# Optimization experiments

Measured on AMD Instinct MI355X. Metric: run time of the kernel, lower is better.

The kernel has to match this reference:

```python
import jax, jax.numpy as jnp
import numpy as np

TAU = 0.5   # init tau
BN_EPS = 1e-5


def _mlp(x, W1, b1, W2, b2, gamma, beta):
    # NRI MLP: fc -> ELU -> fc -> ELU -> batch-norm over flattened (B*E) rows
    h = jax.nn.elu(x @ W1 + b1)
    h = jax.nn.elu(h @ W2 + b2)
    m = h.mean(axis=(0, 1))
    v = jnp.var(h, axis=(0, 1))
    return gamma * (h - m) * jax.lax.rsqrt(v + BN_EPS) + beta


def setup_inputs() -> dict:
    key = jax.random.key(0)
    B, N, F_IN, FC, H = 16, 128, 8, 256, 256
    E = N * (N - 1)
    ks = jax.random.split(key, 24)

    # fully-connected off-diagonal edge list -> one-hot relation matrices
    pairs = np.array([(i, j) for i in range(N) for j in range(N) if i != j], dtype=np.int64)
    eye = np.eye(N, dtype=np.float32)
    rel_rec = jnp.broadcast_to(jnp.asarray(eye[pairs[:, 0]]), (B, E, N))
    rel_send = jnp.broadcast_to(jnp.asarray(eye[pairs[:, 1]]), (B, E, N))

    graph = jax.random.normal(ks[0], (B, E, F_IN), dtype=jnp.float32)
    u = jax.random.uniform(ks[1], (B, E, F_IN), minval=1e-6, maxval=1.0 - 1e-6)
    gumbel_noise = -jnp.log(-jnp.log(u))

    def lin(k, i, o):
        return jax.random.normal(k, (i, o), dtype=jnp.float32) / np.sqrt(i)

    inp = dict(graph=graph, rel_rec=rel_rec, rel_send=rel_send, gumbel_noise=gumbel_noise,
        m1_W1=lin(ks[2], F_IN, FC), m1_b1=jnp.zeros(FC), m1_W2=lin(ks[3], FC, FC), m1_b2=jnp.zeros(FC),
        m1_g=jnp.ones(FC), m1_beta=jnp.zeros(FC),
        m2_W1=lin(ks[4], FC, FC), m2_b1=jnp.zeros(FC), m2_W2=lin(ks[5], FC, FC), m2_b2=jnp.zeros(FC),
        m2_g=jnp.ones(FC), m2_beta=jnp.zeros(FC),
        Wi=lin(ks[6], 2 * FC, H), bi=jnp.zeros(H), Wn=lin(ks[7], 2 * FC, H), bn_b=jnp.zeros(H),
        f1_W=lin(ks[8], H, H), f1_b=jnp.zeros(H), f2_W=lin(ks[9], H, H), f2_b=jnp.zeros(H),
        f3_W=lin(ks[10], H, F_IN), f3_b=jnp.zeros(F_IN))
    return inp


def reference(graph, rel_rec, rel_send, gumbel_noise,
              m1_W1, m1_b1, m1_W2, m1_b2, m1_g, m1_beta,
              m2_W1, m2_b1, m2_W2, m2_b2, m2_g, m2_beta,
              Wi, bi, Wn, bn_b, f1_W, f1_b, f2_W, f2_b, f3_W, f3_b):
    N = rel_rec.shape[-1]
    # source does graph[:, :, :] = graph[0, 0] (broadcast first edge feature)
    graph = jnp.broadcast_to(graph[0, 0], graph.shape)
    x = _mlp(graph, m1_W1, m1_b1, m1_W2, m1_b2, m1_g, m1_beta)          # [B,E,FC]
    # edge2node: mean aggregation of incoming edges (one-hot matmul == scatter-add / N)
    node = jnp.einsum('ben,bef->bnf', rel_rec, x) / N                    # [B,N,FC]
    node = _mlp(node, m2_W1, m2_b1, m2_W2, m2_b2, m2_g, m2_beta)
    # node2edge: gather receiver/sender node features
    recv = jnp.einsum('ben,bnf->bef', rel_rec, node)
    send = jnp.einsum('ben,bnf->bef', rel_send, node)
    x = jnp.concatenate([recv, send], axis=-1)                           # [B,E,2*FC]
    # GRU-style gated update with zero initial hidden: hidden = (1-i)*n
    i = jax.nn.sigmoid(x @ Wi + bi)
    n = jnp.tanh(x @ Wn + bn_b)
    hidden = (1.0 - i) * n
    o = jax.nn.relu(hidden @ f1_W + f1_b)   # dropout p=0 -> identity
    o = jax.nn.relu(o @ f2_W + f2_b)
    logits = o @ f3_W + f3_b                 # [B,E,n_in] edge-type logits
    prob = jax.nn.softmax(logits, axis=-1)   # custom_softmax
    g_graph = jax.nn.softmax((logits + gumbel_noise) / TAU, axis=-1)  # gumbel_softmax, hard=False
    return (g_graph, prob)
```

## Files before the change

kernel.cpp:

```cpp
#include <hip/hip_runtime.h>


#define FC   256
#define HID  256
#define NOUT 8

#define WS_H  64
#define WS_O1 320
#define WS_O2 576

__global__ __launch_bounds__(256) void gate_cols(
    const float* __restrict__ beta,
    const float* __restrict__ Wi, const float* __restrict__ Wn,
    const float* __restrict__ bi, const float* __restrict__ bn_b,
    float* __restrict__ ws)
{
    const int b  = blockIdx.x;
    const int t  = threadIdx.x;
    const int c0 = b * 4;

    const float ck = beta[t];
    const float4 wi0 = *reinterpret_cast<const float4*>(&Wi[(size_t)t * HID + c0]);
    const float4 wi1 = *reinterpret_cast<const float4*>(&Wi[(size_t)(t + 256) * HID + c0]);
    const float4 wn0 = *reinterpret_cast<const float4*>(&Wn[(size_t)t * HID + c0]);
    const float4 wn1 = *reinterpret_cast<const float4*>(&Wn[(size_t)(t + 256) * HID + c0]);

    float v[8];
    v[0] = ck * (wi0.x + wi1.x); v[1] = ck * (wi0.y + wi1.y);
    v[2] = ck * (wi0.z + wi1.z); v[3] = ck * (wi0.w + wi1.w);
    v[4] = ck * (wn0.x + wn1.x); v[5] = ck * (wn0.y + wn1.y);
    v[6] = ck * (wn0.z + wn1.z); v[7] = ck * (wn0.w + wn1.w);

    #pragma unroll
    for (int off = 32; off > 0; off >>= 1) {
        #pragma unroll
        for (int j = 0; j < 8; ++j) v[j] += __shfl_xor(v[j], off, 64);
    }

    __shared__ float lds[4][8];
    const int lane = t & 63, wid = t >> 6;
    if (lane == 0) {
        #pragma unroll
        for (int j = 0; j < 8; ++j) lds[wid][j] = v[j];
    }
    __syncthreads();
    if (t < 4) {
        const float ai = lds[0][t] + lds[1][t] + lds[2][t] + lds[3][t];
        const float an = lds[0][4 + t] + lds[1][4 + t] + lds[2][4 + t] + lds[3][4 + t];
        const int c = c0 + t;
        const float iv = 1.f / (1.f + expf(-(ai + bi[c])));
        const float nv = tanhf(an + bn_b[c]);
        ws[WS_H + c] = (1.f - iv) * nv;
    }
}

__global__ __launch_bounds__(256) void fc_cols(
    const float* __restrict__ W, const float* __restrict__ bias,
    const float* __restrict__ vin, float* __restrict__ vout)
{
    const int b  = blockIdx.x;
    const int t  = threadIdx.x;
    const int c0 = b * 4;

    const float hv = vin[t];
    const float4 w = *reinterpret_cast<const float4*>(&W[(size_t)t * HID + c0]);
    float v[4] = {hv * w.x, hv * w.y, hv * w.z, hv * w.w};

    #pragma unroll
    for (int off = 32; off > 0; off >>= 1) {
        #pragma unroll
        for (int j = 0; j < 4; ++j) v[j] += __shfl_xor(v[j], off, 64);
    }

    __shared__ float lds[4][4];
    const int lane = t & 63, wid = t >> 6;
    if (lane == 0) {
        #pragma unroll
        for (int j = 0; j < 4; ++j) lds[wid][j] = v[j];
    }
    __syncthreads();
    if (t < 4) {
        const float a = lds[0][t] + lds[1][t] + lds[2][t] + lds[3][t];
        vout[c0 + t] = fmaxf(a + bias[c0 + t], 0.f);
    }
}

__global__ __launch_bounds__(256) void f3_softmax(
    const float* __restrict__ f3W, const float* __restrict__ f3b,
    float* __restrict__ ws)
{
    __shared__ float red[NOUT * 256];
    __shared__ float sL[NOUT];
    const int t = threadIdx.x;

    const float o2 = ws[WS_O2 + t];
    const float4 wlo = *reinterpret_cast<const float4*>(&f3W[(size_t)t * NOUT]);
    const float4 whi = *reinterpret_cast<const float4*>(&f3W[(size_t)t * NOUT + 4]);
    red[0*256+t] = o2*wlo.x; red[1*256+t] = o2*wlo.y;
    red[2*256+t] = o2*wlo.z; red[3*256+t] = o2*wlo.w;
    red[4*256+t] = o2*whi.x; red[5*256+t] = o2*whi.y;
    red[6*256+t] = o2*whi.z; red[7*256+t] = o2*whi.w;
    __syncthreads();
    for (int s = 128; s > 0; s >>= 1) {
        if (t < s) {
            #pragma unroll
            for (int j = 0; j < NOUT; ++j) red[j*256+t] += red[j*256+t+s];
        }
        __syncthreads();
    }
    if (t < NOUT) { sL[t] = red[t * 256] + f3b[t]; ws[t] = sL[t]; }
    __syncthreads();
    if (t == 0) {
        float m = sL[0];
        #pragma unroll
        for (int j = 1; j < NOUT; ++j) m = fmaxf(m, sL[j]);
        float e[NOUT], s = 0.f;
        #pragma unroll
        for (int j = 0; j < NOUT; ++j) { e[j] = expf(sL[j] - m); s += e[j]; }
        const float inv = 1.f / s;
        #pragma unroll
        for (int j = 0; j < NOUT; ++j) ws[NOUT + j] = e[j] * inv;
    }
}

__global__ __launch_bounds__(256) void gumbel_kernel(
    const float* __restrict__ gn,
    const float* __restrict__ ws,
    float* __restrict__ out,
    int rows)
{
    const int r = blockIdx.x * blockDim.x + threadIdx.x;
    if (r >= rows) return;

    float L[NOUT];
    #pragma unroll
    for (int j = 0; j < NOUT; ++j) L[j] = ws[j];

    const float4* gp = reinterpret_cast<const float4*>(gn + (size_t)r * NOUT);
    const float4 g0 = gp[0];
    const float4 g1 = gp[1];
    const float g[NOUT] = {g0.x, g0.y, g0.z, g0.w, g1.x, g1.y, g1.z, g1.w};

    float z[NOUT];
    float m = -1e30f;
    #pragma unroll
    for (int j = 0; j < NOUT; ++j) {
        z[j] = (L[j] + g[j]) * 2.0f;
        m = fmaxf(m, z[j]);
    }
    float s = 0.f;
    #pragma unroll
    for (int j = 0; j < NOUT; ++j) { z[j] = expf(z[j] - m); s += z[j]; }
    const float inv = 1.f / s;

    float4* op = reinterpret_cast<float4*>(out + (size_t)r * NOUT);
    op[0] = make_float4(z[0]*inv, z[1]*inv, z[2]*inv, z[3]*inv);
    op[1] = make_float4(z[4]*inv, z[5]*inv, z[6]*inv, z[7]*inv);

    float4* pp = reinterpret_cast<float4*>(out + (size_t)(rows + r) * NOUT);
    pp[0] = make_float4(ws[8],  ws[9],  ws[10], ws[11]);
    pp[1] = make_float4(ws[12], ws[13], ws[14], ws[15]);
}

extern "C" void kernel_launch(void* const* d_in, const int* in_sizes, int n_in,
                              void* d_out, int out_size, void* d_ws, size_t ws_size,
                              hipStream_t stream) {
    const float* gumbel  = (const float*)d_in[3];
    const float* m2_beta = (const float*)d_in[15];
    const float* Wi      = (const float*)d_in[16];
    const float* bi      = (const float*)d_in[17];
    const float* Wn      = (const float*)d_in[18];
    const float* bn_b    = (const float*)d_in[19];
    const float* f1W     = (const float*)d_in[20];
    const float* f1b     = (const float*)d_in[21];
    const float* f2W     = (const float*)d_in[22];
    const float* f2b     = (const float*)d_in[23];
    const float* f3W     = (const float*)d_in[24];
    const float* f3b     = (const float*)d_in[25];

    const int rows = in_sizes[3] / NOUT;
    float* ws = (float*)d_ws;

    gate_cols<<<64, 256, 0, stream>>>(m2_beta, Wi, Wn, bi, bn_b, ws);
    fc_cols<<<64, 256, 0, stream>>>(f1W, f1b, ws + WS_H,  ws + WS_O1);
    fc_cols<<<64, 256, 0, stream>>>(f2W, f2b, ws + WS_O1, ws + WS_O2);
    f3_softmax<<<1, 256, 0, stream>>>(f3W, f3b, ws);

    const int threads = 256;
    const int blocks = (rows + threads - 1) / threads;
    gumbel_kernel<<<blocks, threads, 0, stream>>>(gumbel, ws, (float*)d_out, rows);
}
```

Before: 23.53 us.

## Fuse head MLP kernels into one cooperative kernel with grid syncs

Merges the gate, two fully-connected, and final softmax kernels into a single cooperative launch of 64 blocks, separated by grid-wide syncs. The goal is to remove three kernel launch gaps on the small serial head computation. In exchange it adds cooperative launch overhead and grid barrier costs, and the final stage runs on only one block while the others idle.

```diff
diff --git a/kernel.cpp b/kernel.cpp
--- a/kernel.cpp
+++ b/kernel.cpp
@@ -1,4 +1,7 @@
 #include <hip/hip_runtime.h>
+#include <hip/hip_cooperative_groups.h>
+
+namespace cg = cooperative_groups;
 
 
 #define FC   256
@@ -9,117 +12,132 @@
 #define WS_O1 320
 #define WS_O2 576
 
-__global__ __launch_bounds__(256) void gate_cols(
+__global__ __launch_bounds__(256) void head_coop(
     const float* __restrict__ beta,
-    const float* __restrict__ Wi, const float* __restrict__ Wn,
-    const float* __restrict__ bi, const float* __restrict__ bn_b,
-    float* __restrict__ ws)
-{
-    const int b  = blockIdx.x;
-    const int t  = threadIdx.x;
-    const int c0 = b * 4;
-
-    const float ck = beta[t];
-    const float4 wi0 = *reinterpret_cast<const float4*>(&Wi[(size_t)t * HID + c0]);
-    const float4 wi1 = *reinterpret_cast<const float4*>(&Wi[(size_t)(t + 256) * HID + c0]);
-    const float4 wn0 = *reinterpret_cast<const float4*>(&Wn[(size_t)t * HID + c0]);
-    const float4 wn1 = *reinterpret_cast<const float4*>(&Wn[(size_t)(t + 256) * HID + c0]);
-
-    float v[8];
-    v[0] = ck * (wi0.x + wi1.x); v[1] = ck * (wi0.y + wi1.y);
-    v[2] = ck * (wi0.z + wi1.z); v[3] = ck * (wi0.w + wi1.w);
-    v[4] = ck * (wn0.x + wn1.x); v[5] = ck * (wn0.y + wn1.y);
-    v[6] = ck * (wn0.z + wn1.z); v[7] = ck * (wn0.w + wn1.w);
-
-    #pragma unroll
-    for (int off = 32; off > 0; off >>= 1) {
-        #pragma unroll
-        for (int j = 0; j < 8; ++j) v[j] += __shfl_xor(v[j], off, 64);
-    }
-
-    __shared__ float lds[4][8];
-    const int lane = t & 63, wid = t >> 6;
-    if (lane == 0) {
-        #pragma unroll
-        for (int j = 0; j < 8; ++j) lds[wid][j] = v[j];
-    }
-    __syncthreads();
-    if (t < 4) {
-        const float ai = lds[0][t] + lds[1][t] + lds[2][t] + lds[3][t];
-        const float an = lds[0][4 + t] + lds[1][4 + t] + lds[2][4 + t] + lds[3][4 + t];
-        const int c = c0 + t;
-        const float iv = 1.f / (1.f + expf(-(ai + bi[c])));
-        const float nv = tanhf(an + bn_b[c]);
-        ws[WS_H + c] = (1.f - iv) * nv;
-    }
-}
-
-__global__ __launch_bounds__(256) void fc_cols(
-    const float* __restrict__ W, const float* __restrict__ bias,
-    const float* __restrict__ vin, float* __restrict__ vout)
-{
-    const int b  = blockIdx.x;
-    const int t  = threadIdx.x;
-    const int c0 = b * 4;
-
-    const float hv = vin[t];
-    const float4 w = *reinterpret_cast<const float4*>(&W[(size_t)t * HID + c0]);
-    float v[4] = {hv * w.x, hv * w.y, hv * w.z, hv * w.w};
-
-    #pragma unroll
-    for (int off = 32; off > 0; off >>= 1) {
-        #pragma unroll
-        for (int j = 0; j < 4; ++j) v[j] += __shfl_xor(v[j], off, 64);
-    }
-
-    __shared__ float lds[4][4];
-    const int lane = t & 63, wid = t >> 6;
-    if (lane == 0) {
-        #pragma unroll
-        for (int j = 0; j < 4; ++j) lds[wid][j] = v[j];
-    }
-    __syncthreads();
-    if (t < 4) {
-        const float a = lds[0][t] + lds[1][t] + lds[2][t] + lds[3][t];
-        vout[c0 + t] = fmaxf(a + bias[c0 + t], 0.f);
-    }
-}
-
-__global__ __launch_bounds__(256) void f3_softmax(
+    const float* __restrict__ Wi, const float* __restrict__ bi,
+    const float* __restrict__ Wn, const float* __restrict__ bn_b,
+    const float* __restrict__ f1W, const float* __restrict__ f1b,
+    const float* __restrict__ f2W, const float* __restrict__ f2b,
     const float* __restrict__ f3W, const float* __restrict__ f3b,
     float* __restrict__ ws)
 {
+    cg::grid_group grid = cg::this_grid();
+    const int b    = blockIdx.x;
+    const int t    = threadIdx.x;
+    const int c0   = b * 4;
+    const int lane = t & 63, wid = t >> 6;
+
+    __shared__ float lds8[4][8];
     __shared__ float red[NOUT * 256];
-    __shared__ float sL[NOUT];
-    const int t = threadIdx.x;
-
-    const float o2 = ws[WS_O2 + t];
-    const float4 wlo = *reinterpret_cast<const float4*>(&f3W[(size_t)t * NOUT]);
-    const float4 whi = *reinterpret_cast<const float4*>(&f3W[(size_t)t * NOUT + 4]);
-    red[0*256+t] = o2*wlo.x; red[1*256+t] = o2*wlo.y;
-    red[2*256+t] = o2*wlo.z; red[3*256+t] = o2*wlo.w;
-    red[4*256+t] = o2*whi.x; red[5*256+t] = o2*whi.y;
-    red[6*256+t] = o2*whi.z; red[7*256+t] = o2*whi.w;
-    __syncthreads();
-    for (int s = 128; s > 0; s >>= 1) {
-        if (t < s) {
-            #pragma unroll
-            for (int j = 0; j < NOUT; ++j) red[j*256+t] += red[j*256+t+s];
-        }
-        __syncthreads();
-    }
-    if (t < NOUT) { sL[t] = red[t * 256] + f3b[t]; ws[t] = sL[t]; }
-    __syncthreads();
-    if (t == 0) {
-        float m = sL[0];
+
+    {
+        const float ck = beta[t];
+        const float4 wi0 = *reinterpret_cast<const float4*>(&Wi[(size_t)t * HID + c0]);
+        const float4 wi1 = *reinterpret_cast<const float4*>(&Wi[(size_t)(t + 256) * HID + c0]);
+        const float4 wn0 = *reinterpret_cast<const float4*>(&Wn[(size_t)t * HID + c0]);
+        const float4 wn1 = *reinterpret_cast<const float4*>(&Wn[(size_t)(t + 256) * HID + c0]);
+        float v[8];
+        v[0]=ck*(wi0.x+wi1.x); v[1]=ck*(wi0.y+wi1.y); v[2]=ck*(wi0.z+wi1.z); v[3]=ck*(wi0.w+wi1.w);
+        v[4]=ck*(wn0.x+wn1.x); v[5]=ck*(wn0.y+wn1.y); v[6]=ck*(wn0.z+wn1.z); v[7]=ck*(wn0.w+wn1.w);
         #pragma unroll
-        for (int j = 1; j < NOUT; ++j) m = fmaxf(m, sL[j]);
-        float e[NOUT], s = 0.f;
+        for (int off = 32; off; off >>= 1) {
+            #pragma unroll
+            for (int j = 0; j < 8; ++j) v[j] += __shfl_xor(v[j], off, 64);
+        }
+        if (lane == 0) {
+            #pragma unroll
+            for (int j = 0; j < 8; ++j) lds8[wid][j] = v[j];
+        }
+        __syncthreads();
+        if (t < 4) {
+            const float ai = lds8[0][t]+lds8[1][t]+lds8[2][t]+lds8[3][t];
+            const float an = lds8[0][4+t]+lds8[1][4+t]+lds8[2][4+t]+lds8[3][4+t];
+            const int c = c0 + t;
+            const float iv = 1.f / (1.f + expf(-(ai + bi[c])));
+            const float nv = tanhf(an + bn_b[c]);
+            ws[WS_H + c] = (1.f - iv) * nv;
+        }
+    }
+    __threadfence();
+    grid.sync();
+
+    {
+        const float hv = ws[WS_H + t];
+        const float4 w = *reinterpret_cast<const float4*>(&f1W[(size_t)t * HID + c0]);
+        float v[4] = {hv*w.x, hv*w.y, hv*w.z, hv*w.w};
         #pragma unroll
-        for (int j = 0; j < NOUT; ++j) { e[j] = expf(sL[j] - m); s += e[j]; }
-        const float inv = 1.f / s;
+        for (int off = 32; off; off >>= 1) {
+            #pragma unroll
+            for (int j = 0; j < 4; ++j) v[j] += __shfl_xor(v[j], off, 64);
+        }
+        if (lane == 0) {
+            #pragma unroll
+            for (int j = 0; j < 4; ++j) lds8[wid][j] = v[j];
+        }
+        __syncthreads();
+        if (t < 4) {
+            const float a = lds8[0][t]+lds8[1][t]+lds8[2][t]+lds8[3][t];
+            ws[WS_O1 + c0 + t] = fmaxf(a + f1b[c0 + t], 0.f);
+        }
+    }
+    __threadfence();
+    grid.sync();
+
+    {
+        const float hv = ws[WS_O1 + t];
+        const float4 w = *reinterpret_cast<const float4*>(&f2W[(size_t)t * HID + c0]);
+        float v[4] = {hv*w.x, hv*w.y, hv*w.z, hv*w.w};
         #pragma unroll
-        for (int j = 0; j < NOUT; ++j) ws[NOUT + j] = e[j] * inv;
+        for (int off = 32; off; off >>= 1) {
+            #pragma unroll
+            for (int j = 0; j < 4; ++j) v[j] += __shfl_xor(v[j], off, 64);
+        }
+        if (lane == 0) {
+            #pragma unroll
+            for (int j = 0; j < 4; ++j) lds8[wid][j] = v[j];
+        }
+        __syncthreads();
+        if (t < 4) {
+            const float a = lds8[0][t]+lds8[1][t]+lds8[2][t]+lds8[3][t];
+            ws[WS_O2 + c0 + t] = fmaxf(a + f2b[c0 + t], 0.f);
+        }
+    }
+    __threadfence();
+    grid.sync();
+
+    if (b == 0) {
+        const float o2 = ws[WS_O2 + t];
+        const float4 wlo = *reinterpret_cast<const float4*>(&f3W[(size_t)t * NOUT]);
+        const float4 whi = *reinterpret_cast<const float4*>(&f3W[(size_t)t * NOUT + 4]);
+        red[0*256+t]=o2*wlo.x; red[1*256+t]=o2*wlo.y;
+        red[2*256+t]=o2*wlo.z; red[3*256+t]=o2*wlo.w;
+        red[4*256+t]=o2*whi.x; red[5*256+t]=o2*whi.y;
+        red[6*256+t]=o2*whi.z; red[7*256+t]=o2*whi.w;
+        __syncthreads();
+        for (int s = 128; s; s >>= 1) {
+            if (t < s) {
+                #pragma unroll
+                for (int j = 0; j < NOUT; ++j) red[j*256+t] += red[j*256+t+s];
+            }
+            __syncthreads();
+        }
+        if (t == 0) {
+            float L[NOUT];
+            #pragma unroll
+            for (int j = 0; j < NOUT; ++j) L[j] = red[j*256] + f3b[j];
+            float m = L[0];
+            #pragma unroll
+            for (int j = 1; j < NOUT; ++j) m = fmaxf(m, L[j]);
+            float e[NOUT], s = 0.f;
+            #pragma unroll
+            for (int j = 0; j < NOUT; ++j) { e[j] = expf(L[j] - m); s += e[j]; }
+            const float inv = 1.f / s;
+            #pragma unroll
+            for (int j = 0; j < NOUT; ++j) {
+                ws[j] = L[j];
+                ws[NOUT + j] = e[j] * inv;
+            }
+        }
     }
 }
 
@@ -181,10 +199,14 @@
     const int rows = in_sizes[3] / NOUT;
     float* ws = (float*)d_ws;
 
-    gate_cols<<<64, 256, 0, stream>>>(m2_beta, Wi, Wn, bi, bn_b, ws);
-    fc_cols<<<64, 256, 0, stream>>>(f1W, f1b, ws + WS_H,  ws + WS_O1);
-    fc_cols<<<64, 256, 0, stream>>>(f2W, f2b, ws + WS_O1, ws + WS_O2);
-    f3_softmax<<<1, 256, 0, stream>>>(f3W, f3b, ws);
+    void* args[] = {
+        (void*)&m2_beta,
+        (void*)&Wi, (void*)&bi, (void*)&Wn, (void*)&bn_b,
+        (void*)&f1W, (void*)&f1b, (void*)&f2W, (void*)&f2b,
+        (void*)&f3W, (void*)&f3b, (void*)&ws,
+    };
+    hipLaunchCooperativeKernel(reinterpret_cast<const void*>(head_coop),
+                               dim3(64), dim3(256), args, 0, stream);
 
     const int threads = 256;
     const int blocks = (rows + threads - 1) / threads;
```

Measured after the change: 75.60 us. +221.2%, slower.
